# Performance work log

Hardware: AMD Instinct MI355X
Metric: run time of the kernel (lower is better)

## Reference

```python
import jax, jax.numpy as jnp
import numpy as np
from jax import lax

IN_DIM, MID_DIM, OUT_DIM, SIZE_EMBED_DIM = 1024, 512, 50, 64
N_POS = 30
B, N = 4, 512
H = MID_DIM // 2  # per-direction LSTM hidden


def _span_size_ids(n):
    ar = jnp.arange(n)
    ids = ar[None, :] - ar[:, None]          # [i,j] = j - i
    ids = jnp.where(ids < -(N_POS // 2), -(N_POS // 2), ids)
    ids = jnp.where(ids >= N_POS // 2, N_POS // 2 - 1, ids) + N_POS // 2
    return ids.astype(jnp.int32)             # values in [0, 29]


def _lstm_dir(x, Wih, Whh, bih, bhh, reverse):
    # x: (B, N, in_dim) -> (B, N, H)
    b = x.shape[0]
    xs = jnp.swapaxes(x, 0, 1)               # (N, B, in)
    init = (jnp.zeros((b, H), x.dtype), jnp.zeros((b, H), x.dtype))

    def step(carry, xt):
        h, c = carry
        g = xt @ Wih.T + h @ Whh.T + (bih + bhh)
        i, f, gg, o = jnp.split(g, 4, axis=-1)
        c = jax.nn.sigmoid(f) * c + jax.nn.sigmoid(i) * jnp.tanh(gg)
        h = jax.nn.sigmoid(o) * jnp.tanh(c)
        return (h, c), h

    _, hs = lax.scan(step, init, xs, reverse=reverse)
    return jnp.swapaxes(hs, 0, 1)


def setup_inputs() -> dict:
    key = jax.random.key(0)
    ks = jax.random.split(key, 16)
    s = 0.02
    d = {
        'input_embeds': jax.random.normal(ks[0], (B, N, IN_DIM), jnp.float32),
        'Wih_f': jax.random.normal(ks[1], (4 * H, IN_DIM)) * s,
        'Whh_f': jax.random.normal(ks[2], (4 * H, H)) * s,
        'bih_f': jnp.zeros((4 * H,)),
        'bhh_f': jnp.zeros((4 * H,)),
        'Wih_b': jax.random.normal(ks[3], (4 * H, IN_DIM)) * s,
        'Whh_b': jax.random.normal(ks[4], (4 * H, H)) * s,
        'bih_b': jnp.zeros((4 * H,)),
        'bhh_b': jnp.zeros((4 * H,)),
        'W_head': jax.random.normal(ks[5], (MID_DIM, MID_DIM)) * s,
        'b_head': jnp.zeros((MID_DIM,)),
        'W_tail': jax.random.normal(ks[6], (MID_DIM, MID_DIM)) * s,
        'b_tail': jnp.zeros((MID_DIM,)),
        'emb_table': jax.random.normal(ks[7], (N_POS, SIZE_EMBED_DIM)) * s,
        'W': jax.random.normal(ks[8], (OUT_DIM, 2 * MID_DIM + SIZE_EMBED_DIM + 2)) * s,
    }
    return d


def reference(input_embeds, Wih_f, Whh_f, bih_f, bhh_f, Wih_b, Whh_b, bih_b, bhh_b,
              W_head, b_head, W_tail, b_tail, emb_table, W):
    n = input_embeds.shape[1]
    # BiLSTM (dropouts are identity at eval)
    h_f = _lstm_dir(input_embeds, Wih_f, Whh_f, bih_f, bhh_f, reverse=False)
    h_b = _lstm_dir(input_embeds, Wih_b, Whh_b, bih_b, bhh_b, reverse=True)
    x = jnp.concatenate([h_f, h_b], axis=-1)              # (B, N, mid)
    head = jax.nn.leaky_relu(x @ W_head.T + b_head)        # (B, N, mid)
    tail = jax.nn.leaky_relu(x @ W_tail.T + b_tail)
    ones = jnp.ones_like(head[..., :1])
    head1 = jnp.concatenate([head, ones], axis=-1)         # (B, N, mid+1)
    tail1 = jnp.concatenate([tail, ones], axis=-1)
    se = emb_table[_span_size_ids(n)]                      # (N, N, se)
    # einsum('bmnh,kh->bkmn', cat([head1_m, tail1_n, se_mn]), W) decomposed:
    mp1 = MID_DIM + 1
    Wh, Wt, Ws = W[:, :mp1], W[:, mp1:2 * mp1], W[:, 2 * mp1:]
    s_head = jnp.einsum('bmh,kh->bkm', head1, Wh)          # (B, k, N)
    s_tail = jnp.einsum('bnh,kh->bkn', tail1, Wt)
    s_size = jnp.einsum('mnh,kh->kmn', se, Ws)             # (k, N, N)
    return s_head[:, :, :, None] + s_tail[:, :, None, :] + s_size[None]
```

## Files before the change

### kernel.cpp

```cpp
#include <hip/hip_runtime.h>
#include <hip/hip_bf16.h>
#include <stdint.h>


typedef float  floatx4 __attribute__((ext_vector_type(4)));
typedef short  short8  __attribute__((ext_vector_type(8)));
typedef int    int4v   __attribute__((ext_vector_type(4)));

#define LOG2E_F  1.4426950408889634f
#define TWOLOG2E_F 2.8853900817779268f

__device__ __forceinline__ short f2bf(float f) {
    __hip_bfloat16 h = __float2bfloat16(f);
    return *reinterpret_cast<short*>(&h);
}
__device__ __forceinline__ float fexp2(float x) {
#if __has_builtin(__builtin_amdgcn_exp2f)
    return __builtin_amdgcn_exp2f(x);
#else
    float r; asm("v_exp_f32 %0, %1" : "=v"(r) : "v"(x)); return r;
#endif
}
__device__ __forceinline__ float frcp(float x) {
#if __has_builtin(__builtin_amdgcn_rcpf)
    return __builtin_amdgcn_rcpf(x);
#else
    float r; asm("v_rcp_f32 %0, %1" : "=v"(r) : "v"(x)); return r;
#endif
}
__device__ __forceinline__ float sigf(float x)  { return 1.0f / (1.0f + __expf(-x)); }
__device__ __forceinline__ float tanhf_(float x){ return 1.0f - 2.0f / (__expf(2.0f * x) + 1.0f); }
__device__ __forceinline__ int q8i(float x) {
    int q = (int)rintf(x);
    return q > 127 ? 127 : (q < -127 ? -127 : q);
}

__global__ __launch_bounds__(256) void prep_k(
    const float* __restrict__ W, const float* __restrict__ emb,
    const float* __restrict__ bih_f, const float* __restrict__ bhh_f,
    const float* __restrict__ bih_b, const float* __restrict__ bhh_b,
    const float* __restrict__ b_head, const float* __restrict__ b_tail,
    float* __restrict__ ssize, float* __restrict__ wcat,
    float* __restrict__ sbias, float* __restrict__ biasc1, float* __restrict__ biasc2)
{
    const int g0 = blockIdx.x * 256 + threadIdx.x;
    const int gs = gridDim.x * 256;
    for (int i = g0; i < 1600; i += gs) {
        int k = i >> 5, pp = i & 31;
        float acc = 0.0f;
        if (pp < 30)
            for (int h = 0; h < 64; ++h)
                acc += W[(size_t)k * 1090 + 1026 + h] * emb[pp * 64 + h];
        ssize[i] = acc;
    }
    for (int i = g0; i < 128 * 512; i += gs) {
        int r = i >> 9, h = i & 511;
        float v = 0.0f;
        if (r < 50)                    v = W[(size_t)r * 1090 + h];
        else if (r >= 64 && r < 114)   v = W[(size_t)(r - 64) * 1090 + 513 + h];
        wcat[i] = v;
    }
    for (int i = g0; i < 128; i += gs) {
        float v = 0.0f;
        if (i < 50)                    v = W[(size_t)i * 1090 + 512];
        else if (i >= 64 && i < 114)   v = W[(size_t)(i - 64) * 1090 + 1025];
        sbias[i] = v;
    }
    for (int i = g0; i < 2048; i += gs)
        biasc1[i] = (i < 1024) ? (bih_f[i] + bhh_f[i]) : (bih_b[i - 1024] + bhh_b[i - 1024]);
    for (int i = g0; i < 1024; i += gs)
        biasc2[i] = (i < 512) ? b_head[i] : b_tail[i - 512];
}

__global__ __launch_bounds__(256) void gemm_bt(
    const void* __restrict__ Aptr, int a_is_bf16, int lda,
    int a_split_n, int a_split_off,
    const float* __restrict__ B0, const float* __restrict__ B1,
    int nsplit, int ldb,
    const float* __restrict__ bias, int K, int mode,
    float* __restrict__ out0, __hip_bfloat16* __restrict__ out1)
{
    __shared__ __align__(16) short As[128][48];
    __shared__ __align__(16) short Bs[64][48];
    const int tid   = threadIdx.x;
    const int nbase = blockIdx.x * 64;
    const int mbase = blockIdx.y * 128;
    const int aoff  = (nbase >= a_split_n) ? a_split_off : 0;
    const float* Bp = (nbase < nsplit) ? (B0 + (size_t)nbase * ldb)
                                       : (B1 + (size_t)(nbase - nsplit) * ldb);
    const int arow = tid >> 1, akq = (tid & 1) * 16;
    const int brow = tid >> 2, bkq = (tid & 3) * 8;
    const int wv = tid >> 6, ln = tid & 63, l15 = ln & 15, quad = ln >> 4;

    floatx4 acc[2][4];
#pragma unroll
    for (int i = 0; i < 2; ++i)
#pragma unroll
        for (int j = 0; j < 4; ++j) acc[i][j] = (floatx4){0.f, 0.f, 0.f, 0.f};

    const int KI = K >> 5;
    for (int kk = 0; kk < KI; ++kk) {
        short8 sa0, sa1, sb;
        if (a_is_bf16) {
            const unsigned short* A = (const unsigned short*)Aptr;
            const unsigned short* p = A + (size_t)(mbase + arow) * lda + aoff + kk * 32 + akq;
            sa0 = *(const short8*)p;
            sa1 = *(const short8*)(p + 8);
        } else {
            const float* A = (const float*)Aptr;
            const float* p = A + (size_t)(mbase + arow) * lda + aoff + kk * 32 + akq;
            floatx4 v0 = *(const floatx4*)p;
            floatx4 v1 = *(const floatx4*)(p + 4);
            floatx4 v2 = *(const floatx4*)(p + 8);
            floatx4 v3 = *(const floatx4*)(p + 12);
            sa0[0]=f2bf(v0[0]); sa0[1]=f2bf(v0[1]); sa0[2]=f2bf(v0[2]); sa0[3]=f2bf(v0[3]);
            sa0[4]=f2bf(v1[0]); sa0[5]=f2bf(v1[1]); sa0[6]=f2bf(v1[2]); sa0[7]=f2bf(v1[3]);
            sa1[0]=f2bf(v2[0]); sa1[1]=f2bf(v2[1]); sa1[2]=f2bf(v2[2]); sa1[3]=f2bf(v2[3]);
            sa1[4]=f2bf(v3[0]); sa1[5]=f2bf(v3[1]); sa1[6]=f2bf(v3[2]); sa1[7]=f2bf(v3[3]);
        }
        {
            const float* pb = Bp + (size_t)brow * ldb + kk * 32 + bkq;
            floatx4 b0 = *(const floatx4*)pb;
            floatx4 b1 = *(const floatx4*)(pb + 4);
            sb[0]=f2bf(b0[0]); sb[1]=f2bf(b0[1]); sb[2]=f2bf(b0[2]); sb[3]=f2bf(b0[3]);
            sb[4]=f2bf(b1[0]); sb[5]=f2bf(b1[1]); sb[6]=f2bf(b1[2]); sb[7]=f2bf(b1[3]);
        }
        __syncthreads();
        *(short8*)&As[arow][akq]     = sa0;
        *(short8*)&As[arow][akq + 8] = sa1;
        *(short8*)&Bs[brow][bkq]     = sb;
        __syncthreads();

        short8 a0 = *(const short8*)&As[wv * 32 + l15][quad * 8];
        short8 a1 = *(const short8*)&As[wv * 32 + 16 + l15][quad * 8];
#pragma unroll
        for (int nt = 0; nt < 4; ++nt) {
            short8 bb = *(const short8*)&Bs[nt * 16 + l15][quad * 8];
            acc[0][nt] = __builtin_amdgcn_mfma_f32_16x16x32_bf16(a0, bb, acc[0][nt], 0, 0, 0);
            acc[1][nt] = __builtin_amdgcn_mfma_f32_16x16x32_bf16(a1, bb, acc[1][nt], 0, 0, 0);
        }
    }

#pragma unroll
    for (int mt = 0; mt < 2; ++mt)
#pragma unroll
        for (int nt = 0; nt < 4; ++nt) {
            const int gc = nbase + nt * 16 + l15;
            const float bv = bias[gc];
#pragma unroll
            for (int r = 0; r < 4; ++r) {
                const int gr = mbase + wv * 32 + mt * 16 + quad * 4 + r;
                float v = acc[mt][nt][r] + bv;
                if (mode == 0) {
                    const int d = gc >> 10, nn = gc & 1023;
                    const int gate = nn >> 8;
                    const int vrow = ((nn & 255) << 2) | gate;
                    const int t = gr & 511, b = gr >> 9;
                    const float gsc = (gate == 2) ? TWOLOG2E_F : -LOG2E_F;
                    out0[(((size_t)d * 512 + t) * 4 + b) * 1024 + vrow] = v * gsc;
                } else if (mode == 1) {
                    v = v < 0.0f ? 0.01f * v : v;
                    out1[(size_t)gr * 1024 + gc] = __float2bfloat16(v);
                } else {
                    out0[(size_t)gr * 128 + gc] = v;
                }
            }
        }
}

__global__ __launch_bounds__(1024) void lstm_k(
    const float* __restrict__ Whh_f, const float* __restrict__ Whh_b,
    const float* __restrict__ xg, __hip_bfloat16* __restrict__ hcat)
{
    const int dir = blockIdx.x;
    const float* Whh = dir ? Whh_b : Whh_f;
    const float* xgd = xg + (size_t)dir * 512 * 4 * 1024;
    __shared__ __align__(16) float sm_lds[1024];
    __shared__ __align__(16) signed char hq[2][4][64][16];
    __shared__ __align__(16) int gexch[16][64][4];
    const int tid = threadIdx.x;
    const int wv = tid >> 6, ln = tid & 63, l15 = ln & 15, quad = ln >> 4;

    for (int v = wv * 64; v < wv * 64 + 64; ++v) {
        const int orig = ((v & 3) << 8) | (v >> 2);
        floatx4 x = *(const floatx4*)(Whh + (size_t)orig * 256 + ln * 4);
        float m = fmaxf(fmaxf(fabsf(x[0]), fabsf(x[1])), fmaxf(fabsf(x[2]), fabsf(x[3])));
#pragma unroll
        for (int off = 32; off; off >>= 1) m = fmaxf(m, __shfl_xor(m, off, 64));
        if (ln == 0) sm_lds[v] = m;
    }
    for (int i = tid; i < 2 * 4 * 64 * 16 / 4; i += 1024) ((int*)hq)[i] = 0;
    __syncthreads();

    int4v afrag[4][4];
#pragma unroll
    for (int tt = 0; tt < 4; ++tt) {
        const int vrow = (wv * 4 + tt) * 16 + l15;
        const int orig = ((vrow & 3) << 8) | (vrow >> 2);
        const float sm = sm_lds[vrow];
        const float inv = sm > 1e-30f ? 127.0f / sm : 0.0f;
#pragma unroll
        for (int kf = 0; kf < 4; ++kf) {
            const float* p = Whh + (size_t)orig * 256 + kf * 64 + quad * 16;
            int4v fr;
#pragma unroll
            for (int j = 0; j < 4; ++j) {
                floatx4 w4 = *(const floatx4*)(p + j * 4);
                int b0 = q8i(w4[0] * inv), b1 = q8i(w4[1] * inv);
                int b2 = q8i(w4[2] * inv), b3 = q8i(w4[3] * inv);
                fr[j] = (b0 & 255) | ((b1 & 255) << 8) | ((b2 & 255) << 16) | (b3 << 24);
            }
            afrag[tt][kf] = fr;
        }
    }

    const int u_mine = wv * 16 + (ln >> 2);
    const int batch  = ln & 3;
    floatx4 scl;
    {
        const float sc = 1.0f / 16129.0f;
        floatx4 s4 = *(const floatx4*)&sm_lds[u_mine * 4];
        scl[0] = s4[0] * (sc * -LOG2E_F);
        scl[1] = s4[1] * (sc * -LOG2E_F);
        scl[2] = s4[2] * (sc *  TWOLOG2E_F);
        scl[3] = s4[3] * (sc * -LOG2E_F);
    }
    signed char* hq_w = &hq[0][u_mine >> 6][(((u_mine >> 4) & 3) << 4) + batch][u_mine & 15];
    const int t0 = dir ? 511 : 0;
    const ptrdiff_t xstep = dir ? -4096 : 4096;
    const ptrdiff_t hstep = dir ? -512 : 512;
    const float* xp = xgd + (size_t)batch * 1024 + u_mine * 4 + (size_t)t0 * 4096;
    __hip_bfloat16* hc_p = hcat + (size_t)batch * 512 * 512 + dir * 256 + u_mine
                                + (size_t)t0 * 512;

    float c = 0.0f;
    __syncthreads();

    floatx4 xg_cur = *(const floatx4*)xp;

#define LSTM_STEP(P)                                                            \
    {                                                                           \
        xp += xstep;                                                            \
        floatx4 xg_next = *(const floatx4*)xp;   \
        int4v acc[4];                                                           \
        _Pragma("unroll")                                                       \
        for (int tt = 0; tt < 4; ++tt) acc[tt] = (int4v){0, 0, 0, 0};           \
        _Pragma("unroll")                                                       \
        for (int kf = 0; kf < 4; ++kf) {                                        \
            int4v bb = *(const int4v*)&hq[P][kf][ln][0];                        \
            _Pragma("unroll")                                                   \
            for (int tt = 0; tt < 4; ++tt)                                      \
                acc[tt] = __builtin_amdgcn_mfma_i32_16x16x64_i8(                \
                    afrag[tt][kf], bb, acc[tt], 0, 0, 0);                       \
        }                                                                       \
        if (l15 < 4) {                                                          \
            _Pragma("unroll")                                                   \
            for (int tt = 0; tt < 4; ++tt)                                      \
                *(int4v*)&gexch[wv][(tt * 4 + quad) * 4 + l15][0] = acc[tt];    \
        }                                                                       \
        int4v g = *(const int4v*)&gexch[wv][ln][0];                             \
        float gi = fmaf((float)g[0], scl[0], xg_cur[0]);                        \
        float gf = fmaf((float)g[1], scl[1], xg_cur[1]);                        \
        float gg = fmaf((float)g[2], scl[2], xg_cur[2]);                        \
        float go = fmaf((float)g[3], scl[3], xg_cur[3]);                        \
        float iv = frcp(1.0f + fexp2(gi));           \
        float fv = frcp(1.0f + fexp2(gf));                                      \
        float tg = fmaf(-2.0f, frcp(1.0f + fexp2(gg)), 1.0f);         \
        float ov = frcp(1.0f + fexp2(go));                                      \
        c = fmaf(fv, c, iv * tg);                                               \
        float tc = fmaf(-2.0f, frcp(1.0f + fexp2(c * TWOLOG2E_F)), 1.0f);       \
        float h = ov * tc;                                                      \
        *hc_p = __float2bfloat16(h);                                            \
        hq_w[(P) ? 0 : 4096] = (signed char)q8i(h * 127.0f);                    \
        hc_p += hstep;                                                          \
        xg_cur = xg_next;                                                       \
        asm volatile("s_waitcnt lgkmcnt(0)" ::: "memory");                      \
        __builtin_amdgcn_s_barrier();                                           \
        __builtin_amdgcn_sched_barrier(0);                                      \
        asm volatile("" ::: "memory");                                          \
    }

    for (int s = 0; s < 512; s += 2) {
        LSTM_STEP(0)
        LSTM_STEP(1)
    }
#undef LSTM_STEP
}

__global__ __launch_bounds__(256) void final_k(
    const float* __restrict__ sarr, const float* __restrict__ ssize,
    float* __restrict__ out)
{
    const int mb = blockIdx.x * 64;
    const int k  = blockIdx.y;
    const int b  = blockIdx.z;
    __shared__ float st[512];
    __shared__ float sh[64];
    __shared__ float ss[32];
    const int tid = threadIdx.x;
    for (int n = tid; n < 512; n += 256)
        st[n] = sarr[((size_t)b * 512 + n) * 128 + 64 + k];
    if (tid < 64) sh[tid] = sarr[((size_t)b * 512 + mb + tid) * 128 + k];
    if (tid < 32) ss[tid] = ssize[k * 32 + tid];
    __syncthreads();
    const int n4 = (tid & 127) * 4;
    const int m0 = tid >> 7;
    float* ob = out + (((size_t)b * 50 + k) * 512 + mb) * 512;
    for (int mi = m0; mi < 64; mi += 2) {
        const int m = mb + mi;
        const float base = sh[mi];
        floatx4 v;
#pragma unroll
        for (int e = 0; e < 4; ++e) {
            int d = n4 + e - m;
            d = d < -15 ? -15 : (d > 14 ? 14 : d);
            v[e] = base + st[n4 + e] + ss[d + 15];
        }
        *(floatx4*)(ob + (size_t)mi * 512 + n4) = v;
    }
}

extern "C" void kernel_launch(void* const* d_in, const int* in_sizes, int n_in,
                              void* d_out, int out_size, void* d_ws, size_t ws_size,
                              hipStream_t stream)
{
    const float* input_embeds = (const float*)d_in[0];
    const float* Wih_f  = (const float*)d_in[1];
    const float* Whh_f  = (const float*)d_in[2];
    const float* bih_f  = (const float*)d_in[3];
    const float* bhh_f  = (const float*)d_in[4];
    const float* Wih_b  = (const float*)d_in[5];
    const float* Whh_b  = (const float*)d_in[6];
    const float* bih_b  = (const float*)d_in[7];
    const float* bhh_b  = (const float*)d_in[8];
    const float* W_head = (const float*)d_in[9];
    const float* b_head = (const float*)d_in[10];
    const float* W_tail = (const float*)d_in[11];
    const float* b_tail = (const float*)d_in[12];
    const float* emb    = (const float*)d_in[13];
    const float* W      = (const float*)d_in[14];
    float* out = (float*)d_out;

    char* w = (char*)d_ws;
    float* xg     = (float*)w;  w += (size_t)2 * 512 * 4 * 1024 * 4;
    float* biasc1 = (float*)w;  w += 2048 * 4;
    float* biasc2 = (float*)w;  w += 1024 * 4;
    float* sbias  = (float*)w;  w += 128 * 4;
    float* ssize  = (float*)w;  w += 1600 * 4;
    float* wcat   = (float*)w;  w += 65536 * 4;
    float* sarr   = (float*)w;  w += 262144 * 4;
    __hip_bfloat16* hcat = (__hip_bfloat16*)w;  w += (size_t)2048 * 512 * 2;
    __hip_bfloat16* ht   = (__hip_bfloat16*)w;  w += (size_t)2048 * 1024 * 2;

    hipLaunchKernelGGL(prep_k, dim3(64), dim3(256), 0, stream,
        W, emb, bih_f, bhh_f, bih_b, bhh_b, b_head, b_tail,
        ssize, wcat, sbias, biasc1, biasc2);

    hipLaunchKernelGGL(gemm_bt, dim3(32, 16), dim3(256), 0, stream,
        (const void*)input_embeds, 0, 1024, 1 << 30, 0,
        Wih_f, Wih_b, 1024, 1024, biasc1, 1024, 0, xg, (__hip_bfloat16*)nullptr);

    hipLaunchKernelGGL(lstm_k, dim3(2), dim3(1024), 0, stream, Whh_f, Whh_b, xg, hcat);

    hipLaunchKernelGGL(gemm_bt, dim3(16, 16), dim3(256), 0, stream,
        (const void*)hcat, 1, 512, 1 << 30, 0,
        W_head, W_tail, 512, 512, biasc2, 512, 1, (float*)nullptr, ht);

    hipLaunchKernelGGL(gemm_bt, dim3(2, 16), dim3(256), 0, stream,
        (const void*)ht, 1, 1024, 64, 512,
        wcat, wcat, 1 << 30, 512, sbias, 512, 2, sarr, (__hip_bfloat16*)nullptr);

    hipLaunchKernelGGL(final_k, dim3(8, 50, 4), dim3(256), 0, stream, sarr, ssize, out);
}
```

Measured before the change: 882.7 us.

## Pre-convert GEMM operands to bf16 in prep kernel and restructure LSTM MFMA chain

Moves all fp32-to-bf16 conversion of the input, the Wih weights, the head/tail weights and the final weight slice into the prep kernel, so every GEMM launch loads bf16 operands directly instead of converting per tile. The workspace is repacked to alias buffers whose lifetimes do not overlap. In the LSTM step the four hidden-state fragments are loaded up front, each gate tile's MFMA chain starts from a zero accumulator, the x-gate prefetch uses ping-pong registers instead of a copy, and the int8 quantisation clamp is dropped. The prep kernel now streams about 10 MB of extra conversion traffic on only 64 blocks, which may cost more than it saves, since the serial LSTM kernel likely dominates the total time.

```diff
diff --git a/kernel.cpp b/kernel.cpp
--- a/kernel.cpp
+++ b/kernel.cpp
@@ -4,6 +4,7 @@
 
 
 typedef float  floatx4 __attribute__((ext_vector_type(4)));
+typedef short  short4v __attribute__((ext_vector_type(4)));
 typedef short  short8  __attribute__((ext_vector_type(8)));
 typedef int    int4v   __attribute__((ext_vector_type(4)));
 
@@ -28,23 +29,61 @@
     float r; asm("v_rcp_f32 %0, %1" : "=v"(r) : "v"(x)); return r;
 #endif
 }
-__device__ __forceinline__ float sigf(float x)  { return 1.0f / (1.0f + __expf(-x)); }
-__device__ __forceinline__ float tanhf_(float x){ return 1.0f - 2.0f / (__expf(2.0f * x) + 1.0f); }
 __device__ __forceinline__ int q8i(float x) {
     int q = (int)rintf(x);
     return q > 127 ? 127 : (q < -127 ? -127 : q);
 }
 
 __global__ __launch_bounds__(256) void prep_k(
+    const float* __restrict__ input_embeds,
+    const float* __restrict__ Wih_f, const float* __restrict__ Wih_b,
+    const float* __restrict__ W_head, const float* __restrict__ W_tail,
     const float* __restrict__ W, const float* __restrict__ emb,
     const float* __restrict__ bih_f, const float* __restrict__ bhh_f,
     const float* __restrict__ bih_b, const float* __restrict__ bhh_b,
     const float* __restrict__ b_head, const float* __restrict__ b_tail,
-    float* __restrict__ ssize, float* __restrict__ wcat,
-    float* __restrict__ sbias, float* __restrict__ biasc1, float* __restrict__ biasc2)
+    float* __restrict__ ssize, float* __restrict__ sbias,
+    float* __restrict__ biasc1, float* __restrict__ biasc2,
+    __hip_bfloat16* __restrict__ abf, __hip_bfloat16* __restrict__ wihbf,
+    __hip_bfloat16* __restrict__ wc2bf, __hip_bfloat16* __restrict__ wcbf)
 {
     const int g0 = blockIdx.x * 256 + threadIdx.x;
     const int gs = gridDim.x * 256;
+
+    for (int i4 = g0; i4 < (2048 * 1024) / 4; i4 += gs) {
+        floatx4 v = *(const floatx4*)(input_embeds + (size_t)i4 * 4);
+        short4v s = { f2bf(v[0]), f2bf(v[1]), f2bf(v[2]), f2bf(v[3]) };
+        *(short4v*)(abf + (size_t)i4 * 4) = s;
+    }
+    for (int i4 = g0; i4 < (2048 * 1024) / 4; i4 += gs) {
+        int r = i4 >> 8, c4 = (i4 & 255) * 4;
+        const float* src = (r < 1024) ? (Wih_f + (size_t)r * 1024 + c4)
+                                      : (Wih_b + (size_t)(r - 1024) * 1024 + c4);
+        floatx4 v = *(const floatx4*)src;
+        short4v s = { f2bf(v[0]), f2bf(v[1]), f2bf(v[2]), f2bf(v[3]) };
+        *(short4v*)(wihbf + (size_t)i4 * 4) = s;
+    }
+    for (int i4 = g0; i4 < (1024 * 512) / 4; i4 += gs) {
+        int r = i4 >> 7, c4 = (i4 & 127) * 4;
+        const float* src = (r < 512) ? (W_head + (size_t)r * 512 + c4)
+                                     : (W_tail + (size_t)(r - 512) * 512 + c4);
+        floatx4 v = *(const floatx4*)src;
+        short4v s = { f2bf(v[0]), f2bf(v[1]), f2bf(v[2]), f2bf(v[3]) };
+        *(short4v*)(wc2bf + (size_t)i4 * 4) = s;
+    }
+    for (int i4 = g0; i4 < (128 * 512) / 4; i4 += gs) {
+        int r = i4 >> 7, c4 = (i4 & 127) * 4;
+        short4v s = {0, 0, 0, 0};
+        if (r < 50) {
+            const float* p = W + (size_t)r * 1090 + c4;
+            s[0] = f2bf(p[0]); s[1] = f2bf(p[1]); s[2] = f2bf(p[2]); s[3] = f2bf(p[3]);
+        } else if (r >= 64 && r < 114) {
+            const float* p = W + (size_t)(r - 64) * 1090 + 513 + c4;
+            s[0] = f2bf(p[0]); s[1] = f2bf(p[1]); s[2] = f2bf(p[2]); s[3] = f2bf(p[3]);
+        }
+        *(short4v*)(wcbf + (size_t)i4 * 4) = s;
+    }
+
     for (int i = g0; i < 1600; i += gs) {
         int k = i >> 5, pp = i & 31;
         float acc = 0.0f;
@@ -53,13 +92,6 @@
                 acc += W[(size_t)k * 1090 + 1026 + h] * emb[pp * 64 + h];
         ssize[i] = acc;
     }
-    for (int i = g0; i < 128 * 512; i += gs) {
-        int r = i >> 9, h = i & 511;
-        float v = 0.0f;
-        if (r < 50)                    v = W[(size_t)r * 1090 + h];
-        else if (r >= 64 && r < 114)   v = W[(size_t)(r - 64) * 1090 + 513 + h];
-        wcat[i] = v;
-    }
     for (int i = g0; i < 128; i += gs) {
         float v = 0.0f;
         if (i < 50)                    v = W[(size_t)i * 1090 + 512];
@@ -73,10 +105,9 @@
 }
 
 __global__ __launch_bounds__(256) void gemm_bt(
-    const void* __restrict__ Aptr, int a_is_bf16, int lda,
+    const __hip_bfloat16* __restrict__ Abf, int lda,
     int a_split_n, int a_split_off,
-    const float* __restrict__ B0, const float* __restrict__ B1,
-    int nsplit, int ldb,
+    const __hip_bfloat16* __restrict__ Bbf, int ldb,
     const float* __restrict__ bias, int K, int mode,
     float* __restrict__ out0, __hip_bfloat16* __restrict__ out1)
 {
@@ -86,8 +117,6 @@
     const int nbase = blockIdx.x * 64;
     const int mbase = blockIdx.y * 128;
     const int aoff  = (nbase >= a_split_n) ? a_split_off : 0;
-    const float* Bp = (nbase < nsplit) ? (B0 + (size_t)nbase * ldb)
-                                       : (B1 + (size_t)(nbase - nsplit) * ldb);
     const int arow = tid >> 1, akq = (tid & 1) * 16;
     const int brow = tid >> 2, bkq = (tid & 3) * 8;
     const int wv = tid >> 6, ln = tid & 63, l15 = ln & 15, quad = ln >> 4;
@@ -98,33 +127,16 @@
 #pragma unroll
         for (int j = 0; j < 4; ++j) acc[i][j] = (floatx4){0.f, 0.f, 0.f, 0.f};
 
+    const unsigned short* A = (const unsigned short*)Abf;
+    const unsigned short* B = (const unsigned short*)Bbf;
     const int KI = K >> 5;
     for (int kk = 0; kk < KI; ++kk) {
-        short8 sa0, sa1, sb;
-        if (a_is_bf16) {
-            const unsigned short* A = (const unsigned short*)Aptr;
-            const unsigned short* p = A + (size_t)(mbase + arow) * lda + aoff + kk * 32 + akq;
-            sa0 = *(const short8*)p;
-            sa1 = *(const short8*)(p + 8);
-        } else {
-            const float* A = (const float*)Aptr;
-            const float* p = A + (size_t)(mbase + arow) * lda + aoff + kk * 32 + akq;
-            floatx4 v0 = *(const floatx4*)p;
-            floatx4 v1 = *(const floatx4*)(p + 4);
-            floatx4 v2 = *(const floatx4*)(p + 8);
-            floatx4 v3 = *(const floatx4*)(p + 12);
-            sa0[0]=f2bf(v0[0]); sa0[1]=f2bf(v0[1]); sa0[2]=f2bf(v0[2]); sa0[3]=f2bf(v0[3]);
-            sa0[4]=f2bf(v1[0]); sa0[5]=f2bf(v1[1]); sa0[6]=f2bf(v1[2]); sa0[7]=f2bf(v1[3]);
-            sa1[0]=f2bf(v2[0]); sa1[1]=f2bf(v2[1]); sa1[2]=f2bf(v2[2]); sa1[3]=f2bf(v2[3]);
-            sa1[4]=f2bf(v3[0]); sa1[5]=f2bf(v3[1]); sa1[6]=f2bf(v3[2]); sa1[7]=f2bf(v3[3]);
-        }
-        {
-            const float* pb = Bp + (size_t)brow * ldb + kk * 32 + bkq;
-            floatx4 b0 = *(const floatx4*)pb;
-            floatx4 b1 = *(const floatx4*)(pb + 4);
-            sb[0]=f2bf(b0[0]); sb[1]=f2bf(b0[1]); sb[2]=f2bf(b0[2]); sb[3]=f2bf(b0[3]);
-            sb[4]=f2bf(b1[0]); sb[5]=f2bf(b1[1]); sb[6]=f2bf(b1[2]); sb[7]=f2bf(b1[3]);
-        }
+        const unsigned short* pa = A + (size_t)(mbase + arow) * lda + aoff + kk * 32 + akq;
+        short8 sa0 = *(const short8*)pa;
+        short8 sa1 = *(const short8*)(pa + 8);
+        const unsigned short* pb = B + (size_t)(nbase + brow) * ldb + kk * 32 + bkq;
+        short8 sb = *(const short8*)pb;
+
         __syncthreads();
         *(short8*)&As[arow][akq]     = sa0;
         *(short8*)&As[arow][akq + 8] = sa1;
@@ -234,24 +246,31 @@
                                 + (size_t)t0 * 512;
 
     float c = 0.0f;
+    const int4v z4 = {0, 0, 0, 0};
     __syncthreads();
 
-    floatx4 xg_cur = *(const floatx4*)xp;
-
-#define LSTM_STEP(P)                                                            \
+    floatx4 xga = *(const floatx4*)xp;
+    floatx4 xgb;
+
+#define LSTM_STEP(P, XC, XN)                                                    \
     {                                                                           \
         xp += xstep;                                                            \
-        floatx4 xg_next = *(const floatx4*)xp;   \
+        XN = *(const floatx4*)xp;   \
+        int4v bb0 = *(const int4v*)&hq[P][0][ln][0];                            \
+        int4v bb1 = *(const int4v*)&hq[P][1][ln][0];                            \
+        int4v bb2 = *(const int4v*)&hq[P][2][ln][0];                            \
+        int4v bb3 = *(const int4v*)&hq[P][3][ln][0];                            \
         int4v acc[4];                                                           \
         _Pragma("unroll")                                                       \
-        for (int tt = 0; tt < 4; ++tt) acc[tt] = (int4v){0, 0, 0, 0};           \
-        _Pragma("unroll")                                                       \
-        for (int kf = 0; kf < 4; ++kf) {                                        \
-            int4v bb = *(const int4v*)&hq[P][kf][ln][0];                        \
-            _Pragma("unroll")                                                   \
-            for (int tt = 0; tt < 4; ++tt)                                      \
-                acc[tt] = __builtin_amdgcn_mfma_i32_16x16x64_i8(                \
-                    afrag[tt][kf], bb, acc[tt], 0, 0, 0);                       \
+        for (int tt = 0; tt < 4; ++tt) {                                        \
+            int4v t0v = __builtin_amdgcn_mfma_i32_16x16x64_i8(                  \
+                afrag[tt][0], bb0, z4, 0, 0, 0);                                \
+            t0v = __builtin_amdgcn_mfma_i32_16x16x64_i8(                        \
+                afrag[tt][1], bb1, t0v, 0, 0, 0);                               \
+            t0v = __builtin_amdgcn_mfma_i32_16x16x64_i8(                        \
+                afrag[tt][2], bb2, t0v, 0, 0, 0);                               \
+            acc[tt] = __builtin_amdgcn_mfma_i32_16x16x64_i8(                    \
+                afrag[tt][3], bb3, t0v, 0, 0, 0);                               \
         }                                                                       \
         if (l15 < 4) {                                                          \
             _Pragma("unroll")                                                   \
@@ -259,10 +278,10 @@
                 *(int4v*)&gexch[wv][(tt * 4 + quad) * 4 + l15][0] = acc[tt];    \
         }                                                                       \
         int4v g = *(const int4v*)&gexch[wv][ln][0];                             \
-        float gi = fmaf((float)g[0], scl[0], xg_cur[0]);                        \
-        float gf = fmaf((float)g[1], scl[1], xg_cur[1]);                        \
-        float gg = fmaf((float)g[2], scl[2], xg_cur[2]);                        \
-        float go = fmaf((float)g[3], scl[3], xg_cur[3]);                        \
+        float gi = fmaf((float)g[0], scl[0], XC[0]);                            \
+        float gf = fmaf((float)g[1], scl[1], XC[1]);                            \
+        float gg = fmaf((float)g[2], scl[2], XC[2]);                            \
+        float go = fmaf((float)g[3], scl[3], XC[3]);                            \
         float iv = frcp(1.0f + fexp2(gi));           \
         float fv = frcp(1.0f + fexp2(gf));                                      \
         float tg = fmaf(-2.0f, frcp(1.0f + fexp2(gg)), 1.0f);         \
@@ -271,9 +290,8 @@
         float tc = fmaf(-2.0f, frcp(1.0f + fexp2(c * TWOLOG2E_F)), 1.0f);       \
         float h = ov * tc;                                                      \
         *hc_p = __float2bfloat16(h);                                            \
-        hq_w[(P) ? 0 : 4096] = (signed char)q8i(h * 127.0f);                    \
+        hq_w[(P) ? 0 : 4096] = (signed char)(int)rintf(h * 127.0f);  \
         hc_p += hstep;                                                          \
-        xg_cur = xg_next;                                                       \
         asm volatile("s_waitcnt lgkmcnt(0)" ::: "memory");                      \
         __builtin_amdgcn_s_barrier();                                           \
         __builtin_amdgcn_sched_barrier(0);                                      \
@@ -281,8 +299,8 @@
     }
 
     for (int s = 0; s < 512; s += 2) {
-        LSTM_STEP(0)
-        LSTM_STEP(1)
+        LSTM_STEP(0, xga, xgb)
+        LSTM_STEP(1, xgb, xga)
     }
 #undef LSTM_STEP
 }
@@ -347,28 +365,32 @@
     float* biasc2 = (float*)w;  w += 1024 * 4;
     float* sbias  = (float*)w;  w += 128 * 4;
     float* ssize  = (float*)w;  w += 1600 * 4;
-    float* wcat   = (float*)w;  w += 65536 * 4;
-    float* sarr   = (float*)w;  w += 262144 * 4;
-    __hip_bfloat16* hcat = (__hip_bfloat16*)w;  w += (size_t)2048 * 512 * 2;
-    __hip_bfloat16* ht   = (__hip_bfloat16*)w;  w += (size_t)2048 * 1024 * 2;
+    __hip_bfloat16* wcbf  = (__hip_bfloat16*)w;  w += (size_t)128 * 512 * 2;
+    __hip_bfloat16* wihbf = (__hip_bfloat16*)w;  w += (size_t)2048 * 1024 * 2;
+    __hip_bfloat16* hcat  = (__hip_bfloat16*)w;  w += (size_t)2048 * 512 * 2;
+    float* sarr = (float*)w;
+    __hip_bfloat16* wc2bf = (__hip_bfloat16*)w;  w += (size_t)1024 * 512 * 2;
+    __hip_bfloat16* abf   = (__hip_bfloat16*)w;
+    __hip_bfloat16* ht    = (__hip_bfloat16*)w;  w += (size_t)2048 * 1024 * 2;
 
     hipLaunchKernelGGL(prep_k, dim3(64), dim3(256), 0, stream,
-        W, emb, bih_f, bhh_f, bih_b, bhh_b, b_head, b_tail,
-        ssize, wcat, sbias, biasc1, biasc2);
+        input_embeds, Wih_f, Wih_b, W_head, W_tail, W, emb,
+        bih_f, bhh_f, bih_b, bhh_b, b_head, b_tail,
+        ssize, sbias, biasc1, biasc2, abf, wihbf, wc2bf, wcbf);
 
     hipLaunchKernelGGL(gemm_bt, dim3(32, 16), dim3(256), 0, stream,
-        (const void*)input_embeds, 0, 1024, 1 << 30, 0,
-        Wih_f, Wih_b, 1024, 1024, biasc1, 1024, 0, xg, (__hip_bfloat16*)nullptr);
+        abf, 1024, 1 << 30, 0,
+        wihbf, 1024, biasc1, 1024, 0, xg, (__hip_bfloat16*)nullptr);
 
     hipLaunchKernelGGL(lstm_k, dim3(2), dim3(1024), 0, stream, Whh_f, Whh_b, xg, hcat);
 
     hipLaunchKernelGGL(gemm_bt, dim3(16, 16), dim3(256), 0, stream,
-        (const void*)hcat, 1, 512, 1 << 30, 0,
-        W_head, W_tail, 512, 512, biasc2, 512, 1, (float*)nullptr, ht);
+        hcat, 512, 1 << 30, 0,
+        wc2bf, 512, biasc2, 512, 1, (float*)nullptr, ht);
 
     hipLaunchKernelGGL(gemm_bt, dim3(2, 16), dim3(256), 0, stream,
-        (const void*)ht, 1, 1024, 64, 512,
-        wcat, wcat, 1 << 30, 512, sbias, 512, 2, sarr, (__hip_bfloat16*)nullptr);
+        ht, 1024, 64, 512,
+        wcbf, 512, sbias, 512, 2, sarr, (__hip_bfloat16*)nullptr);
 
     hipLaunchKernelGGL(final_k, dim3(8, 50, 4), dim3(256), 0, stream, sarr, ssize, out);
 }
```

New measurement: 859.9 us. 2.6% less time.
